# Optimization experiments

Measured on AMD Instinct MI355X. Metric: run time of the kernel, lower is better.

## Reference

```python
import jax, jax.numpy as jnp
import numpy as np

D = 768      # model dim
H = 12       # heads
HD = D // H  # head dim
FF = 3072    # mlp hidden = 4*D
EPS = 1e-5   # torch LayerNorm default eps


def setup_inputs() -> dict:
    key = jax.random.key(0)
    ks = jax.random.split(key, 8)
    init = lambda k, shp: (jax.random.normal(k, shp, jnp.float32) * 0.02)
    return {
        "x1": jax.random.normal(ks[0], (8, 512, D), jnp.float32),
        "x2": jax.random.normal(ks[1], (8, 1024, D), jnp.float32),
        "ln1_g": jnp.ones((D,), jnp.float32),
        "ln1_b": jnp.zeros((D,), jnp.float32),
        "w_qkv": init(ks[2], (D, 3 * D)),
        "b_qkv": jnp.zeros((3 * D,), jnp.float32),
        "w_proj": init(ks[3], (D, D)),
        "b_proj": jnp.zeros((D,), jnp.float32),
        "ls1": jnp.full((D,), 1e-5, jnp.float32),
        "ln2_g": jnp.ones((D,), jnp.float32),
        "ln2_b": jnp.zeros((D,), jnp.float32),
        "w_fc1": init(ks[4], (D, FF)),
        "b_fc1": jnp.zeros((FF,), jnp.float32),
        "w_fc2": init(ks[5], (FF, D)),
        "b_fc2": jnp.zeros((D,), jnp.float32),
        "ls2": jnp.full((D,), 1e-5, jnp.float32),
    }


def _ln(x, g, b):
    m = x.mean(-1, keepdims=True)
    v = ((x - m) ** 2).mean(-1, keepdims=True)
    return (x - m) * jax.lax.rsqrt(v + EPS) * g + b


def _block(x, ln1_g, ln1_b, w_qkv, b_qkv, w_proj, b_proj, ls1,
           ln2_g, ln2_b, w_fc1, b_fc1, w_fc2, b_fc2, ls2):
    # Block-diagonal attention over same-length group == independent per-sequence MHA.
    b, n, _ = x.shape
    h = _ln(x, ln1_g, ln1_b)
    qkv = h @ w_qkv + b_qkv                       # [b, n, 3D]
    q, k, v = [t.reshape(b, n, H, HD).transpose(0, 2, 1, 3)
               for t in jnp.split(qkv, 3, axis=-1)]
    scores = jnp.einsum('bhqd,bhkd->bhqk', q, k) * (HD ** -0.5)
    attn = jax.nn.softmax(scores, axis=-1)
    o = jnp.einsum('bhqk,bhkd->bhqd', attn, v).transpose(0, 2, 1, 3).reshape(b, n, D)
    x = x + ls1 * (o @ w_proj + b_proj)           # LayerScale + residual
    h2 = _ln(x, ln2_g, ln2_b)
    mlp = jax.nn.gelu(h2 @ w_fc1 + b_fc1, approximate=False) @ w_fc2 + b_fc2
    return x + ls2 * mlp


def reference(x1, x2, ln1_g, ln1_b, w_qkv, b_qkv, w_proj, b_proj, ls1,
              ln2_g, ln2_b, w_fc1, b_fc1, w_fc2, b_fc2, ls2):
    params = (ln1_g, ln1_b, w_qkv, b_qkv, w_proj, b_proj, ls1,
              ln2_g, ln2_b, w_fc1, b_fc1, w_fc2, b_fc2, ls2)
    y1 = _block(x1, *params)
    y2 = _block(x2, *params)
    # concatenated varlen token stream, equivalent to pre-split cat tensor
    return jnp.concatenate([y1.reshape(-1, D), y2.reshape(-1, D)], axis=0)
```

## Files before the change

### kernel.cpp

```cpp
#include <hip/hip_runtime.h>
#include <hip/hip_bf16.h>
#include <math.h>

typedef __hip_bfloat16 bf16_t;
typedef __bf16 bf16x8 __attribute__((ext_vector_type(8)));
typedef float f32x4 __attribute__((ext_vector_type(4)));
typedef long long ll2 __attribute__((ext_vector_type(2)));
typedef short short8v __attribute__((ext_vector_type(8)));

__device__ __forceinline__ void load_lds16(const void* g, void* l) {
    __builtin_amdgcn_global_load_lds(
        (__attribute__((address_space(1))) void*)g,
        (__attribute__((address_space(3))) void*)l, 16, 0, 0);
}

__device__ __forceinline__ unsigned char f32_fp8(float x) {
    return (unsigned char)(__builtin_amdgcn_cvt_pk_fp8_f32(x, 0.f, 0, false) & 0xff);
}

__device__ __forceinline__ int kperm(int k) {
    return (k & ~63) | (((k >> 3) & 3) << 4) | (((k >> 5) & 1) << 3) | (k & 7);
}

__global__ __launch_bounds__(256) void wconv_kernel(
    const float* __restrict__ W, unsigned char* __restrict__ Wt, int K, int N)
{
    __shared__ float tile[32][33];
    const int k0 = blockIdx.x * 32, n0 = blockIdx.y * 32;
    const int tx = threadIdx.x & 31, ty = threadIdx.x >> 5;
    #pragma unroll
    for (int i = 0; i < 32; i += 8)
        tile[ty + i][tx] = W[(size_t)(k0 + ty + i) * N + n0 + tx];
    __syncthreads();
    #pragma unroll
    for (int i = 0; i < 32; i += 8)
        Wt[(size_t)(n0 + ty + i) * K + kperm(k0 + tx)] = f32_fp8(tile[tx][ty + i] * 64.f);
}

__global__ __launch_bounds__(256) void ln_kernel(
    const float* __restrict__ x0, const float* __restrict__ x1, int split,
    const float* __restrict__ g, const float* __restrict__ b,
    unsigned char* __restrict__ out)
{
    const int t = blockIdx.x;
    const int tid = threadIdx.x;
    const float* xr = (t < split) ? x0 + (size_t)t * 768
                                  : x1 + (size_t)(t - split) * 768;
    float v[3], s = 0.f, q = 0.f;
    #pragma unroll
    for (int i = 0; i < 3; ++i) {
        v[i] = xr[tid + i * 256];
        s += v[i]; q += v[i] * v[i];
    }
    #pragma unroll
    for (int o = 32; o > 0; o >>= 1) {
        s += __shfl_down(s, o);
        q += __shfl_down(q, o);
    }
    __shared__ float rs_[4], rq_[4];
    const int w = tid >> 6, lane = tid & 63;
    if (lane == 0) { rs_[w] = s; rq_[w] = q; }
    __syncthreads();
    s = rs_[0] + rs_[1] + rs_[2] + rs_[3];
    q = rq_[0] + rq_[1] + rq_[2] + rq_[3];
    const float mean = s * (1.f / 768.f);
    const float var  = q * (1.f / 768.f) - mean * mean;
    const float rstd = rsqrtf(var + 1e-5f);
    unsigned char* orow = out + (size_t)t * 768;
    #pragma unroll
    for (int i = 0; i < 3; ++i) {
        const int d = tid + i * 256;
        orow[kperm(d)] = f32_fp8((v[i] - mean) * rstd * g[d] + b[d]);
    }
}

__global__ __launch_bounds__(256) void gemm_kernel(
    const unsigned char* __restrict__ A, const unsigned char* __restrict__ Bt,
    const float* __restrict__ bias, const float* __restrict__ ls,
    const float* __restrict__ resid0, const float* __restrict__ resid1, int rsplit,
    void* __restrict__ outp, bf16_t* __restrict__ vtout,
    int M, int N, int K, int mode)
{
    __shared__ __align__(16) unsigned char As[128 * 64];
    __shared__ __align__(16) unsigned char Bs[128 * 64];
    const int tid  = threadIdx.x;
    const int lane = tid & 63;
    const int w    = tid >> 6;
    const int wm   = w >> 1, wn = w & 1;
    const int l4   = lane & 15, quad = lane >> 4;
    const int bm   = blockIdx.x, bn = blockIdx.y;

    f32x4 acc[4][4];
    #pragma unroll
    for (int i = 0; i < 4; ++i)
        #pragma unroll
        for (int j = 0; j < 4; ++j)
            #pragma unroll
            for (int e = 0; e < 4; ++e) acc[i][j][e] = 0.f;

    const int srow = lane >> 2;
    const int scol = (lane & 3) * 16;
    const unsigned char* Ag = A  + (size_t)(bm * 128) * K;
    const unsigned char* Bg = Bt + (size_t)(bn * 128) * K;

    for (int k0 = 0; k0 < K; k0 += 64) {
        #pragma unroll
        for (int p = 0; p < 2; ++p) {
            const int r = w * 32 + p * 16 + srow;
            load_lds16(Ag + (size_t)r * K + k0 + scol, &As[(w * 32 + p * 16) * 64]);
            load_lds16(Bg + (size_t)r * K + k0 + scol, &Bs[(w * 32 + p * 16) * 64]);
        }
        __syncthreads();
        long af[4][2], bfr[4][2];
        #pragma unroll
        for (int i = 0; i < 4; ++i) {
            const ll2 t = *(const ll2*)&As[(wm * 64 + i * 16 + l4) * 64 + quad * 16];
            af[i][0] = t[0]; af[i][1] = t[1];
        }
        #pragma unroll
        for (int j = 0; j < 4; ++j) {
            const ll2 t = *(const ll2*)&Bs[(wn * 64 + j * 16 + l4) * 64 + quad * 16];
            bfr[j][0] = t[0]; bfr[j][1] = t[1];
        }
        #pragma unroll
        for (int c = 0; c < 2; ++c)
            #pragma unroll
            for (int i = 0; i < 4; ++i)
                #pragma unroll
                for (int j = 0; j < 4; ++j)
                    acc[i][j] = __builtin_amdgcn_mfma_f32_16x16x32_fp8_fp8(
                        af[i][c], bfr[j][c], acc[i][j], 0, 0, 0);
        __syncthreads();
    }

    const float inv64 = 0.015625f;
    #pragma unroll
    for (int i = 0; i < 4; ++i) {
        #pragma unroll
        for (int j = 0; j < 4; ++j) {
            const int col  = bn * 128 + wn * 64 + j * 16 + l4;
            const int row0 = bm * 128 + wm * 64 + i * 16 + quad * 4;
            const float bc = bias[col];
            if (mode == 3) {
                if (bn < 12) {
                    const float sc = (bn < 6) ? 0.125f : 1.f;
                    #pragma unroll
                    for (int r = 0; r < 4; ++r)
                        ((bf16_t*)outp)[(size_t)(row0 + r) * 1536 + col] =
                            __float2bfloat16((acc[i][j][r] * inv64 + bc) * sc);
                } else {
                    bf16_t tmp[4];
                    #pragma unroll
                    for (int r = 0; r < 4; ++r)
                        tmp[r] = __float2bfloat16(acc[i][j][r] * inv64 + bc);
                    *(float2*)(vtout + (size_t)(col - 1536) * 12288 + row0) =
                        *(const float2*)tmp;
                }
            } else if (mode == 1) {
                const int pcol = kperm(col);
                #pragma unroll
                for (int r = 0; r < 4; ++r) {
                    const float v = acc[i][j][r] * inv64 + bc;
                    const float gl = v / (1.f + __expf(-1.702f * v));
                    ((unsigned char*)outp)[(size_t)(row0 + r) * N + pcol] = f32_fp8(gl);
                }
            } else {
                #pragma unroll
                for (int r = 0; r < 4; ++r) {
                    const int row = row0 + r;
                    const float v = acc[i][j][r] * inv64 + bc;
                    const float rv = (row < rsplit)
                        ? resid0[(size_t)row * N + col]
                        : resid1[(size_t)(row - rsplit) * N + col];
                    ((float*)outp)[(size_t)row * N + col] = rv + ls[col] * v;
                }
            }
        }
    }
}

__global__ __launch_bounds__(256) void attn_kernel(
    const bf16_t* __restrict__ qk, const bf16_t* __restrict__ vt,
    unsigned char* __restrict__ ao, int N, int tok_off)
{
    __shared__ __align__(16) bf16_t Qs[64 * 64];
    __shared__ __align__(16) bf16_t Kd[2][64 * 64];
    __shared__ __align__(16) bf16_t Vd[2][64 * 64];
    __shared__ __align__(16) bf16_t Ps[4 * 16 * 72];
    const int qt = blockIdx.x, h = blockIdx.y, s = blockIdx.z;
    const int tid = threadIdx.x, lane = tid & 63, w = tid >> 6;
    const int l4 = lane & 15, quad = lane >> 4;
    const int seq0 = tok_off + s * N;
    const int hoff = h * 64;
    const int lrow = lane >> 3;
    const int lcol = (((lane & 7) ^ (lrow & 7)) * 8);
    const int nkt = N >> 6;
    const int sw = l4 & 7;
    const int c0 = (quad ^ sw) * 8;
    const int c1 = ((quad + 4) ^ sw) * 8;

    #pragma unroll
    for (int p = 0; p < 2; ++p) {
        const int rr = w * 16 + p * 8;
        load_lds16(qk + (size_t)(seq0 + qt * 64 + rr + lrow) * 1536 + hoff + lcol,
                   &Qs[rr * 64]);
    }

    auto stageKV = [&](int kt, int buf) {
        #pragma unroll
        for (int p = 0; p < 2; ++p) {
            const int rr = w * 16 + p * 8;
            load_lds16(qk + (size_t)(seq0 + kt * 64 + rr + lrow) * 1536 + 768 + hoff + lcol,
                       &Kd[buf][rr * 64]);
            load_lds16(vt + (size_t)(hoff + rr + lrow) * 12288 + seq0 + kt * 64 + lcol,
                       &Vd[buf][rr * 64]);
        }
    };
    stageKV(0, 0);

    bf16x8 bones;
    {
        short8v t = {0x3F80, 0x3F80, 0x3F80, 0x3F80, 0x3F80, 0x3F80, 0x3F80, 0x3F80};
        __builtin_memcpy(&bones, &t, 16);
    }

    f32x4 oacc[4], lacc;
    #pragma unroll
    for (int j = 0; j < 4; ++j)
        #pragma unroll
        for (int e = 0; e < 4; ++e) oacc[j][e] = 0.f;
    #pragma unroll
    for (int e = 0; e < 4; ++e) lacc[e] = 0.f;

    bf16_t* Pw = &Ps[w * 16 * 72];

    for (int kt = 0; kt < nkt; ++kt) {
        const int buf = kt & 1;
        __syncthreads();
        if (kt + 1 < nkt) stageKV(kt + 1, buf ^ 1);

        f32x4 st[4];
        #pragma unroll
        for (int j = 0; j < 4; ++j)
            #pragma unroll
            for (int e = 0; e < 4; ++e) st[j][e] = 0.f;
        const bf16x8 aq0 = *(const bf16x8*)&Qs[(w * 16 + l4) * 64 + c0];
        const bf16x8 aq1 = *(const bf16x8*)&Qs[(w * 16 + l4) * 64 + c1];
        #pragma unroll
        for (int j = 0; j < 4; ++j) {
            const bf16x8 b0 = *(const bf16x8*)&Kd[buf][(j * 16 + l4) * 64 + c0];
            const bf16x8 b1 = *(const bf16x8*)&Kd[buf][(j * 16 + l4) * 64 + c1];
            st[j] = __builtin_amdgcn_mfma_f32_16x16x32_bf16(aq0, b0, st[j], 0, 0, 0);
            st[j] = __builtin_amdgcn_mfma_f32_16x16x32_bf16(aq1, b1, st[j], 0, 0, 0);
        }

        #pragma unroll
        for (int j = 0; j < 4; ++j)
            #pragma unroll
            for (int r = 0; r < 4; ++r)
                Pw[(quad * 4 + r) * 72 + j * 16 + l4] =
                    __float2bfloat16(__expf(st[j][r]));

        const bf16x8 ap0 = *(const bf16x8*)&Pw[l4 * 72 + quad * 8];
        const bf16x8 ap1 = *(const bf16x8*)&Pw[l4 * 72 + 32 + quad * 8];
        lacc = __builtin_amdgcn_mfma_f32_16x16x32_bf16(ap0, bones, lacc, 0, 0, 0);
        lacc = __builtin_amdgcn_mfma_f32_16x16x32_bf16(ap1, bones, lacc, 0, 0, 0);
        #pragma unroll
        for (int j = 0; j < 4; ++j) {
            const bf16x8 v0 = *(const bf16x8*)&Vd[buf][(j * 16 + l4) * 64 + c0];
            const bf16x8 v1 = *(const bf16x8*)&Vd[buf][(j * 16 + l4) * 64 + c1];
            oacc[j] = __builtin_amdgcn_mfma_f32_16x16x32_bf16(ap0, v0, oacc[j], 0, 0, 0);
            oacc[j] = __builtin_amdgcn_mfma_f32_16x16x32_bf16(ap1, v1, oacc[j], 0, 0, 0);
        }
    }

    unsigned char* Ps8 = (unsigned char*)Ps;
    #pragma unroll
    for (int r = 0; r < 4; ++r) {
        const float inv = 1.f / lacc[r];
        #pragma unroll
        for (int j = 0; j < 4; ++j)
            Ps8[(w * 16 + quad * 4 + r) * 64 + j * 16 + l4] =
                f32_fp8(oacc[j][r] * inv);
    }
    __syncthreads();
    #pragma unroll
    for (int p = 0; p < 2; ++p) {
        const int idx = p * 256 + tid;
        const int row = idx >> 3, j = idx & 7;
        const int pj = ((j & 3) << 4) | ((j >> 2) << 3);
        *(unsigned long long*)(ao + (size_t)(seq0 + qt * 64 + row) * 768 + hoff + pj) =
            *(const unsigned long long*)&Ps8[row * 64 + j * 8];
    }
}

extern "C" void kernel_launch(void* const* d_in, const int* in_sizes, int n_in,
                              void* d_out, int out_size, void* d_ws, size_t ws_size,
                              hipStream_t stream)
{
    const float* x1     = (const float*)d_in[0];
    const float* x2     = (const float*)d_in[1];
    const float* ln1_g  = (const float*)d_in[2];
    const float* ln1_b  = (const float*)d_in[3];
    const float* w_qkv  = (const float*)d_in[4];
    const float* b_qkv  = (const float*)d_in[5];
    const float* w_proj = (const float*)d_in[6];
    const float* b_proj = (const float*)d_in[7];
    const float* ls1    = (const float*)d_in[8];
    const float* ln2_g  = (const float*)d_in[9];
    const float* ln2_b  = (const float*)d_in[10];
    const float* w_fc1  = (const float*)d_in[11];
    const float* b_fc1  = (const float*)d_in[12];
    const float* w_fc2  = (const float*)d_in[13];
    const float* b_fc2  = (const float*)d_in[14];
    const float* ls2    = (const float*)d_in[15];

    char* ws = (char*)d_ws;
    unsigned char* wqkv_t  = (unsigned char*)(ws + 0);
    unsigned char* wproj_t = (unsigned char*)(ws + 1769472);
    unsigned char* wfc1_t  = (unsigned char*)(ws + 2359296);
    unsigned char* wfc2_t  = (unsigned char*)(ws + 4718592);
    unsigned char* hbuf    = (unsigned char*)(ws + 7077888);
    bf16_t*        qkbuf   = (bf16_t*)(ws + 16515072);
    bf16_t*        vtbuf   = (bf16_t*)(ws + 54263808);
    unsigned char* hidbuf  = (unsigned char*)(ws + 16515072);
    unsigned char* aobuf   = (unsigned char*)(ws + 73138176);
    float*         xr      = (float*)(ws + 82575360);

    wconv_kernel<<<dim3(24, 72), 256, 0, stream>>>(w_qkv,  wqkv_t,  768, 2304);
    wconv_kernel<<<dim3(24, 24), 256, 0, stream>>>(w_proj, wproj_t, 768, 768);
    wconv_kernel<<<dim3(24, 96), 256, 0, stream>>>(w_fc1,  wfc1_t,  768, 3072);
    wconv_kernel<<<dim3(96, 24), 256, 0, stream>>>(w_fc2,  wfc2_t,  3072, 768);

    ln_kernel<<<12288, 256, 0, stream>>>(x1, x2, 4096, ln1_g, ln1_b, hbuf);

    gemm_kernel<<<dim3(96, 18), 256, 0, stream>>>(hbuf, wqkv_t, b_qkv, nullptr,
                                                  nullptr, nullptr, 0,
                                                  qkbuf, vtbuf, 12288, 2304, 768, 3);

    attn_kernel<<<dim3(8, 12, 8), 256, 0, stream>>>(qkbuf, vtbuf, aobuf, 512, 0);
    attn_kernel<<<dim3(16, 12, 8), 256, 0, stream>>>(qkbuf, vtbuf, aobuf, 1024, 4096);

    gemm_kernel<<<dim3(96, 6), 256, 0, stream>>>(aobuf, wproj_t, b_proj, ls1,
                                                 x1, x2, 4096,
                                                 xr, nullptr, 12288, 768, 768, 2);

    ln_kernel<<<12288, 256, 0, stream>>>(xr, xr, 1 << 30, ln2_g, ln2_b, hbuf);

    gemm_kernel<<<dim3(96, 24), 256, 0, stream>>>(hbuf, wfc1_t, b_fc1, nullptr,
                                                  nullptr, nullptr, 0,
                                                  hidbuf, nullptr, 12288, 3072, 768, 1);

    gemm_kernel<<<dim3(96, 6), 256, 0, stream>>>(hidbuf, wfc2_t, b_fc2, ls2,
                                                 xr, xr, 1 << 30,
                                                 (float*)d_out, nullptr, 12288, 768, 3072, 2);
}
```

Measured before the change: 450.8 us.

## Switch FP8 GEMM to 32x32x64 scaled MFMA with rotated LDS layout

Replaces the 16x16x32 FP8 MFMA tiling with the gfx950 32x32x64 f8f6f4 scaled MFMA, using unit scales. This removes the K-permutation previously applied by the weight conversion, LayerNorm and attention output writers. A per-row chunk rotation is applied when loading into LDS so fragment reads avoid bank conflicts. The epilogue is remapped to the 32x32 accumulator layout. The intent is fewer MFMA issues and fewer LDS reads per K step, at the cost of a different register layout and new correctness risk in the fragment mapping.

```diff
diff --git a/kernel.cpp b/kernel.cpp
--- a/kernel.cpp
+++ b/kernel.cpp
@@ -5,7 +5,9 @@
 typedef __hip_bfloat16 bf16_t;
 typedef __bf16 bf16x8 __attribute__((ext_vector_type(8)));
 typedef float f32x4 __attribute__((ext_vector_type(4)));
-typedef long long ll2 __attribute__((ext_vector_type(2)));
+typedef float f32x16 __attribute__((ext_vector_type(16)));
+typedef int int32x8 __attribute__((ext_vector_type(8)));
+typedef int int4v __attribute__((ext_vector_type(4)));
 typedef short short8v __attribute__((ext_vector_type(8)));
 
 __device__ __forceinline__ void load_lds16(const void* g, void* l) {
@@ -18,10 +20,6 @@
     return (unsigned char)(__builtin_amdgcn_cvt_pk_fp8_f32(x, 0.f, 0, false) & 0xff);
 }
 
-__device__ __forceinline__ int kperm(int k) {
-    return (k & ~63) | (((k >> 3) & 3) << 4) | (((k >> 5) & 1) << 3) | (k & 7);
-}
-
 __global__ __launch_bounds__(256) void wconv_kernel(
     const float* __restrict__ W, unsigned char* __restrict__ Wt, int K, int N)
 {
@@ -34,7 +32,7 @@
     __syncthreads();
     #pragma unroll
     for (int i = 0; i < 32; i += 8)
-        Wt[(size_t)(n0 + ty + i) * K + kperm(k0 + tx)] = f32_fp8(tile[tx][ty + i] * 64.f);
+        Wt[(size_t)(n0 + ty + i) * K + k0 + tx] = f32_fp8(tile[tx][ty + i] * 64.f);
 }
 
 __global__ __launch_bounds__(256) void ln_kernel(
@@ -70,8 +68,19 @@
     #pragma unroll
     for (int i = 0; i < 3; ++i) {
         const int d = tid + i * 256;
-        orow[kperm(d)] = f32_fp8((v[i] - mean) * rstd * g[d] + b[d]);
-    }
+        orow[d] = f32_fp8((v[i] - mean) * rstd * g[d] + b[d]);
+    }
+}
+
+__device__ __forceinline__ int32x8 frag32(const unsigned char* S, int row, int lh) {
+    const int rot = (row >> 1) & 3;
+    const int t0 = lh * 2;
+    const int4v lo = *(const int4v*)&S[row * 64 + (((t0 + rot) & 3) << 4)];
+    const int4v hi = *(const int4v*)&S[row * 64 + (((t0 + 1 + rot) & 3) << 4)];
+    int32x8 r;
+    r[0] = lo[0]; r[1] = lo[1]; r[2] = lo[2]; r[3] = lo[3];
+    r[4] = hi[0]; r[5] = hi[1]; r[6] = hi[2]; r[7] = hi[3];
+    return r;
 }
 
 __global__ __launch_bounds__(256) void gemm_kernel(
@@ -87,19 +96,19 @@
     const int lane = tid & 63;
     const int w    = tid >> 6;
     const int wm   = w >> 1, wn = w & 1;
-    const int l4   = lane & 15, quad = lane >> 4;
+    const int l32  = lane & 31, lh = lane >> 5;
     const int bm   = blockIdx.x, bn = blockIdx.y;
 
-    f32x4 acc[4][4];
-    #pragma unroll
-    for (int i = 0; i < 4; ++i)
-        #pragma unroll
-        for (int j = 0; j < 4; ++j)
+    f32x16 acc[2][2];
+    #pragma unroll
+    for (int i = 0; i < 2; ++i)
+        #pragma unroll
+        for (int j = 0; j < 2; ++j)
             #pragma unroll
-            for (int e = 0; e < 4; ++e) acc[i][j][e] = 0.f;
-
-    const int srow = lane >> 2;
-    const int scol = (lane & 3) * 16;
+            for (int e = 0; e < 16; ++e) acc[i][j][e] = 0.f;
+
+    const int srow   = lane >> 2;
+    const int schunk = lane & 3;
     const unsigned char* Ag = A  + (size_t)(bm * 128) * K;
     const unsigned char* Bg = Bt + (size_t)(bn * 128) * K;
 
@@ -107,73 +116,78 @@
         #pragma unroll
         for (int p = 0; p < 2; ++p) {
             const int r = w * 32 + p * 16 + srow;
-            load_lds16(Ag + (size_t)r * K + k0 + scol, &As[(w * 32 + p * 16) * 64]);
-            load_lds16(Bg + (size_t)r * K + k0 + scol, &Bs[(w * 32 + p * 16) * 64]);
+            const int gc = ((schunk - ((r >> 1) & 3)) & 3) * 16;
+            load_lds16(Ag + (size_t)r * K + k0 + gc, &As[(w * 32 + p * 16) * 64]);
+            load_lds16(Bg + (size_t)r * K + k0 + gc, &Bs[(w * 32 + p * 16) * 64]);
         }
         __syncthreads();
-        long af[4][2], bfr[4][2];
-        #pragma unroll
-        for (int i = 0; i < 4; ++i) {
-            const ll2 t = *(const ll2*)&As[(wm * 64 + i * 16 + l4) * 64 + quad * 16];
-            af[i][0] = t[0]; af[i][1] = t[1];
-        }
-        #pragma unroll
-        for (int j = 0; j < 4; ++j) {
-            const ll2 t = *(const ll2*)&Bs[(wn * 64 + j * 16 + l4) * 64 + quad * 16];
-            bfr[j][0] = t[0]; bfr[j][1] = t[1];
-        }
-        #pragma unroll
-        for (int c = 0; c < 2; ++c)
+        int32x8 af[2], bf2[2];
+        #pragma unroll
+        for (int i = 0; i < 2; ++i)
+            af[i] = frag32(As, wm * 64 + i * 32 + l32, lh);
+        #pragma unroll
+        for (int j = 0; j < 2; ++j)
+            bf2[j] = frag32(Bs, wn * 64 + j * 32 + l32, lh);
+        #pragma unroll
+        for (int i = 0; i < 2; ++i)
             #pragma unroll
-            for (int i = 0; i < 4; ++i)
-                #pragma unroll
-                for (int j = 0; j < 4; ++j)
-                    acc[i][j] = __builtin_amdgcn_mfma_f32_16x16x32_fp8_fp8(
-                        af[i][c], bfr[j][c], acc[i][j], 0, 0, 0);
+            for (int j = 0; j < 2; ++j)
+                acc[i][j] = __builtin_amdgcn_mfma_scale_f32_32x32x64_f8f6f4(
+                    af[i], bf2[j], acc[i][j], 0, 0,
+                    0, 0x7F7F7F7F, 0, 0x7F7F7F7F);
         __syncthreads();
     }
 
     const float inv64 = 0.015625f;
     #pragma unroll
-    for (int i = 0; i < 4; ++i) {
-        #pragma unroll
-        for (int j = 0; j < 4; ++j) {
-            const int col  = bn * 128 + wn * 64 + j * 16 + l4;
-            const int row0 = bm * 128 + wm * 64 + i * 16 + quad * 4;
+    for (int i = 0; i < 2; ++i) {
+        #pragma unroll
+        for (int j = 0; j < 2; ++j) {
+            const int col  = bn * 128 + wn * 64 + j * 32 + l32;
+            const int rowb = bm * 128 + wm * 64 + i * 32 + 4 * lh;
             const float bc = bias[col];
             if (mode == 3) {
                 if (bn < 12) {
                     const float sc = (bn < 6) ? 0.125f : 1.f;
                     #pragma unroll
-                    for (int r = 0; r < 4; ++r)
-                        ((bf16_t*)outp)[(size_t)(row0 + r) * 1536 + col] =
-                            __float2bfloat16((acc[i][j][r] * inv64 + bc) * sc);
+                    for (int g = 0; g < 4; ++g)
+                        #pragma unroll
+                        for (int r = 0; r < 4; ++r)
+                            ((bf16_t*)outp)[(size_t)(rowb + 8 * g + r) * 1536 + col] =
+                                __float2bfloat16((acc[i][j][4 * g + r] * inv64 + bc) * sc);
                 } else {
-                    bf16_t tmp[4];
                     #pragma unroll
-                    for (int r = 0; r < 4; ++r)
-                        tmp[r] = __float2bfloat16(acc[i][j][r] * inv64 + bc);
-                    *(float2*)(vtout + (size_t)(col - 1536) * 12288 + row0) =
-                        *(const float2*)tmp;
+                    for (int g = 0; g < 4; ++g) {
+                        bf16_t tmp[4];
+                        #pragma unroll
+                        for (int r = 0; r < 4; ++r)
+                            tmp[r] = __float2bfloat16(acc[i][j][4 * g + r] * inv64 + bc);
+                        *(float2*)(vtout + (size_t)(col - 1536) * 12288 + rowb + 8 * g) =
+                            *(const float2*)tmp;
+                    }
                 }
             } else if (mode == 1) {
-                const int pcol = kperm(col);
                 #pragma unroll
-                for (int r = 0; r < 4; ++r) {
-                    const float v = acc[i][j][r] * inv64 + bc;
-                    const float gl = v / (1.f + __expf(-1.702f * v));
-                    ((unsigned char*)outp)[(size_t)(row0 + r) * N + pcol] = f32_fp8(gl);
-                }
+                for (int g = 0; g < 4; ++g)
+                    #pragma unroll
+                    for (int r = 0; r < 4; ++r) {
+                        const float v = acc[i][j][4 * g + r] * inv64 + bc;
+                        const float gl = v / (1.f + __expf(-1.702f * v));
+                        ((unsigned char*)outp)[(size_t)(rowb + 8 * g + r) * N + col] =
+                            f32_fp8(gl);
+                    }
             } else {
                 #pragma unroll
-                for (int r = 0; r < 4; ++r) {
-                    const int row = row0 + r;
-                    const float v = acc[i][j][r] * inv64 + bc;
-                    const float rv = (row < rsplit)
-                        ? resid0[(size_t)row * N + col]
-                        : resid1[(size_t)(row - rsplit) * N + col];
-                    ((float*)outp)[(size_t)row * N + col] = rv + ls[col] * v;
-                }
+                for (int g = 0; g < 4; ++g)
+                    #pragma unroll
+                    for (int r = 0; r < 4; ++r) {
+                        const int row = rowb + 8 * g + r;
+                        const float v = acc[i][j][4 * g + r] * inv64 + bc;
+                        const float rv = (row < rsplit)
+                            ? resid0[(size_t)row * N + col]
+                            : resid1[(size_t)(row - rsplit) * N + col];
+                        ((float*)outp)[(size_t)row * N + col] = rv + ls[col] * v;
+                    }
             }
         }
     }
@@ -288,8 +302,7 @@
     for (int p = 0; p < 2; ++p) {
         const int idx = p * 256 + tid;
         const int row = idx >> 3, j = idx & 7;
-        const int pj = ((j & 3) << 4) | ((j >> 2) << 3);
-        *(unsigned long long*)(ao + (size_t)(seq0 + qt * 64 + row) * 768 + hoff + pj) =
+        *(unsigned long long*)(ao + (size_t)(seq0 + qt * 64 + row) * 768 + hoff + j * 8) =
             *(const unsigned long long*)&Ps8[row * 64 + j * 8];
     }
 }
```

New measurement: 417.5 us. 7.4% less time.
